# Kernel tuning notes

Measured on AMD Instinct MI355X. Metric: run time of the kernel, lower is better.

The kernel has to match this reference:

```python
import jax, jax.numpy as jnp
import numpy as np

N_NODES = 20000
N_EDGES = 640000
IN_FEATS = 128
H1, H2 = 64, 32


def setup_inputs() -> dict:
    key = jax.random.key(0)
    ks = jax.random.split(key, 7)
    features = jax.random.normal(ks[0], (N_NODES, IN_FEATS), dtype=jnp.float32)
    W1 = jax.random.normal(ks[1], (IN_FEATS, H1), dtype=jnp.float32) * (1.0 / np.sqrt(IN_FEATS))
    b1 = jax.random.normal(ks[2], (H1,), dtype=jnp.float32) * 0.01
    W2 = jax.random.normal(ks[3], (H1, H2), dtype=jnp.float32) * (1.0 / np.sqrt(H1))
    b2 = jax.random.normal(ks[4], (H2,), dtype=jnp.float32) * 0.01
    src = jax.random.randint(ks[5], (N_EDGES,), 0, N_NODES, dtype=jnp.int32)
    dst = jax.random.randint(ks[6], (N_EDGES,), 0, N_NODES, dtype=jnp.int32)
    return {"features": features, "W1": W1, "b1": b1, "W2": W2, "b2": b2,
            "src": src, "dst": dst}


def _gcn_aggregate(h, src, dst, n_nodes):
    # copy_u + sum: gather source-node features along edges, sum at destinations
    return jax.ops.segment_sum(h[src], dst, num_segments=n_nodes)


def reference(features, W1, b1, W2, b2, src, dst):
    n = features.shape[0]
    # layer 1: aggregate then linear, relu
    h = _gcn_aggregate(features, src, dst, n)          # [N, in_feats]
    x = jax.nn.relu(h @ W1 + b1)                       # [N, 64]
    # layer 2: aggregate then linear
    h2 = _gcn_aggregate(x, src, dst, n)                # [N, 64]
    return h2 @ W2 + b2                                # [N, 32]
```

## Files before the change

### kernel.cpp

```cpp
#include <hip/hip_runtime.h>


#define NF 128
#define H1 64
#define H2 32
#define CAP 128
#define CAPSH 7
#define NG8 8
#define FILL_BPG 80

__device__ __forceinline__ float blo(unsigned u) { return __uint_as_float(u << 16); }
__device__ __forceinline__ float bhi(unsigned u) { return __uint_as_float(u & 0xffff0000u); }
__device__ __forceinline__ unsigned short f2b(float f) {
    unsigned x = __float_as_uint(f);
    return (unsigned short)((x + 0x7fffu + ((x >> 16) & 1u)) >> 16);
}

__launch_bounds__(256)
__global__ void gemm1_kernel(const float* __restrict__ F, const float* __restrict__ W1,
                             unsigned short* __restrict__ P1b, int* __restrict__ cntz,
                             int n_zero, int n_nodes) {
    int idx = blockIdx.x * 256 + threadIdx.x;
    if (idx < n_zero) cntz[idx] = 0;
    __shared__ float w[NF][H1];
    const float4* w4 = (const float4*)W1;
    float4* ws4 = (float4*)&w[0][0];
#pragma unroll
    for (int j = 0; j < 8; ++j) ws4[threadIdx.x + 256 * j] = w4[threadIdx.x + 256 * j];
    __syncthreads();
    int wid = threadIdx.x >> 6, lane = threadIdx.x & 63;
#pragma unroll
    for (int r = 0; r < 8; ++r) {
        int row = blockIdx.x * 32 + wid * 8 + r;
        if (row >= n_nodes) break;
        const float4* f4 = (const float4*)(F + (size_t)row * NF);
        float acc = 0.f;
#pragma unroll
        for (int k4 = 0; k4 < NF / 4; ++k4) {
            float4 fv = f4[k4];
            acc += fv.x * w[k4 * 4 + 0][lane];
            acc += fv.y * w[k4 * 4 + 1][lane];
            acc += fv.z * w[k4 * 4 + 2][lane];
            acc += fv.w * w[k4 * 4 + 3][lane];
        }
        P1b[(size_t)row * H1 + lane] = f2b(acc);
    }
}

__launch_bounds__(256)
__global__ void stage_kernel(const int* __restrict__ src, const int* __restrict__ dst,
                             unsigned* __restrict__ staged, int* __restrict__ gcur,
                             int n_edges, int sz, int capg) {
    __shared__ int lcnt[NG8];
    __shared__ int lbase[NG8];
    int t = threadIdx.x;
    if (t < NG8) lcnt[t] = 0;
    __syncthreads();
    int i4 = (blockIdx.x * 256 + t) * 4;
    int dd[4], ss[4], bb[4], pp[4];
    if (i4 + 4 <= n_edges) {
        int4 d4 = *(const int4*)(dst + i4);
        int4 s4 = *(const int4*)(src + i4);
        dd[0] = d4.x; dd[1] = d4.y; dd[2] = d4.z; dd[3] = d4.w;
        ss[0] = s4.x; ss[1] = s4.y; ss[2] = s4.z; ss[3] = s4.w;
    } else {
#pragma unroll
        for (int k = 0; k < 4; ++k) {
            int e = i4 + k;
            dd[k] = (e < n_edges) ? dst[e] : -1;
            ss[k] = (e < n_edges) ? src[e] : 0;
        }
    }
#pragma unroll
    for (int k = 0; k < 4; ++k) {
        if (dd[k] >= 0) {
            bb[k] = (unsigned)dd[k] / (unsigned)sz;
            pp[k] = atomicAdd(&lcnt[bb[k]], 1);
        }
    }
    __syncthreads();
    if (t < NG8) lbase[t] = lcnt[t] ? atomicAdd(&gcur[t], lcnt[t]) : 0;
    __syncthreads();
#pragma unroll
    for (int k = 0; k < 4; ++k) {
        if (dd[k] >= 0) {
            int pos = lbase[bb[k]] + pp[k];
            if (pos < capg)
                staged[(size_t)bb[k] * capg + pos] = ((unsigned)dd[k] << 16) | (unsigned)ss[k];
        }
    }
}

__launch_bounds__(256)
__global__ void fill2_kernel(const unsigned* __restrict__ staged, const int* __restrict__ gcur,
                             int* __restrict__ cnt, unsigned short* __restrict__ slots,
                             int capg) {
    int g = blockIdx.x & (NG8 - 1), gi = blockIdx.x >> 3;
    int ecnt = min(gcur[g], capg);
    const unsigned* sg = staged + (size_t)g * capg;
    int stride = FILL_BPG * 256 * 4;
    for (int j = (gi * 256 + threadIdx.x) * 4; j < ecnt; j += stride) {
        if (j + 4 <= ecnt) {
            uint4 u = *(const uint4*)(sg + j);
            int d, p;
            d = u.x >> 16; p = atomicAdd(&cnt[d], 1); if (p < CAP) slots[(d << CAPSH) + p] = (unsigned short)(u.x & 0xffffu);
            d = u.y >> 16; p = atomicAdd(&cnt[d], 1); if (p < CAP) slots[(d << CAPSH) + p] = (unsigned short)(u.y & 0xffffu);
            d = u.z >> 16; p = atomicAdd(&cnt[d], 1); if (p < CAP) slots[(d << CAPSH) + p] = (unsigned short)(u.z & 0xffffu);
            d = u.w >> 16; p = atomicAdd(&cnt[d], 1); if (p < CAP) slots[(d << CAPSH) + p] = (unsigned short)(u.w & 0xffffu);
        } else {
            for (int k = j; k < ecnt; ++k) {
                unsigned u = sg[k];
                int d = u >> 16;
                int p = atomicAdd(&cnt[d], 1);
                if (p < CAP) slots[(d << CAPSH) + p] = (unsigned short)(u & 0xffffu);
            }
        }
    }
}

__launch_bounds__(256)
__global__ void agg1gemm2_kernel(const unsigned short* __restrict__ P1b,
                                 const int* __restrict__ cnt, const unsigned short* __restrict__ slots,
                                 const float* __restrict__ b1, const float* __restrict__ W2,
                                 unsigned short* __restrict__ P2b, int n_nodes, int sz) {
    __shared__ float w[H1][H2];
    __shared__ float arow[4][H1];
    const float4* w4 = (const float4*)W2;
    float4* ws4 = (float4*)&w[0][0];
#pragma unroll
    for (int j = 0; j < 2; ++j) ws4[threadIdx.x + 256 * j] = w4[threadIdx.x + 256 * j];
    __syncthreads();
    int wid = threadIdx.x >> 6, lane = threadIdx.x & 63;
    int g = blockIdx.x & (NG8 - 1), gi = blockIdx.x >> 3;
    int ni = gi * 4 + wid;
    if (ni >= sz) return;
    int node = g * sz + ni;
    if (node >= n_nodes) return;
    int deg = min(cnt[node], CAP);
    int base = node << CAPSH;
    int q = lane >> 4, c = lane & 15;
    const uint2* P1v = (const uint2*)P1b;
    float a0 = 0.f, a1 = 0.f, a2 = 0.f, a3 = 0.f;
    float c0 = 0.f, c1 = 0.f, c2 = 0.f, c3 = 0.f;
    int i = 0;
    for (; i + 8 <= deg; i += 8) {
        int sA = slots[base + i + q];
        int sB = slots[base + i + 4 + q];
        uint2 uA = P1v[(sA << 4) + c];
        uint2 uB = P1v[(sB << 4) + c];
        a0 += blo(uA.x); a1 += bhi(uA.x); a2 += blo(uA.y); a3 += bhi(uA.y);
        c0 += blo(uB.x); c1 += bhi(uB.x); c2 += blo(uB.y); c3 += bhi(uB.y);
    }
    for (; i + 4 <= deg; i += 4) {
        int sA = slots[base + i + q];
        uint2 uA = P1v[(sA << 4) + c];
        a0 += blo(uA.x); a1 += bhi(uA.x); a2 += blo(uA.y); a3 += bhi(uA.y);
    }
    int r = deg - i;
    if (q < r) {
        int sA = slots[base + i + q];
        uint2 uA = P1v[(sA << 4) + c];
        a0 += blo(uA.x); a1 += bhi(uA.x); a2 += blo(uA.y); a3 += bhi(uA.y);
    }
    a0 += c0; a1 += c1; a2 += c2; a3 += c3;
    a0 += __shfl_xor(a0, 16, 64); a0 += __shfl_xor(a0, 32, 64);
    a1 += __shfl_xor(a1, 16, 64); a1 += __shfl_xor(a1, 32, 64);
    a2 += __shfl_xor(a2, 16, 64); a2 += __shfl_xor(a2, 32, 64);
    a3 += __shfl_xor(a3, 16, 64); a3 += __shfl_xor(a3, 32, 64);
    if (q == 0) {
        float4 bb = *(const float4*)(b1 + 4 * c);
        float4 v;
        v.x = fmaxf(a0 + bb.x, 0.f);
        v.y = fmaxf(a1 + bb.y, 0.f);
        v.z = fmaxf(a2 + bb.z, 0.f);
        v.w = fmaxf(a3 + bb.w, 0.f);
        *(float4*)&arow[wid][4 * c] = v;
    }
    int half = lane >> 5, c32 = lane & 31;
    int kb = half * 32;
    float acc2 = 0.f;
#pragma unroll
    for (int k = 0; k < 32; ++k) acc2 += arow[wid][kb + k] * w[kb + k][c32];
    acc2 += __shfl_xor(acc2, 32, 64);
    if (lane < 32) P2b[(size_t)node * H2 + c32] = f2b(acc2);
}

__launch_bounds__(256)
__global__ void agg2_kernel(const unsigned short* __restrict__ P2b,
                            const int* __restrict__ cnt, const unsigned short* __restrict__ slots,
                            const float* __restrict__ b2, float* __restrict__ out,
                            int n_nodes, int sz) {
    int wid = threadIdx.x >> 6, lane = threadIdx.x & 63;
    int g = blockIdx.x & (NG8 - 1), gi = blockIdx.x >> 3;
    int ni = gi * 4 + wid;
    if (ni >= sz) return;
    int node = g * sz + ni;
    if (node >= n_nodes) return;
    int deg = min(cnt[node], CAP);
    int base = node << CAPSH;
    int o = lane >> 3, c = lane & 7;
    const uint2* P2v = (const uint2*)P2b;
    float a0 = 0.f, a1 = 0.f, a2 = 0.f, a3 = 0.f;
    float c0 = 0.f, c1 = 0.f, c2 = 0.f, c3 = 0.f;
    int i = 0;
    for (; i + 16 <= deg; i += 16) {
        int sA = slots[base + i + o];
        int sB = slots[base + i + 8 + o];
        uint2 uA = P2v[(sA << 3) + c];
        uint2 uB = P2v[(sB << 3) + c];
        a0 += blo(uA.x); a1 += bhi(uA.x); a2 += blo(uA.y); a3 += bhi(uA.y);
        c0 += blo(uB.x); c1 += bhi(uB.x); c2 += blo(uB.y); c3 += bhi(uB.y);
    }
    for (; i + 8 <= deg; i += 8) {
        int sA = slots[base + i + o];
        uint2 uA = P2v[(sA << 3) + c];
        a0 += blo(uA.x); a1 += bhi(uA.x); a2 += blo(uA.y); a3 += bhi(uA.y);
    }
    int r = deg - i;
    if (o < r) {
        int sA = slots[base + i + o];
        uint2 uA = P2v[(sA << 3) + c];
        a0 += blo(uA.x); a1 += bhi(uA.x); a2 += blo(uA.y); a3 += bhi(uA.y);
    }
    a0 += c0; a1 += c1; a2 += c2; a3 += c3;
    a0 += __shfl_xor(a0, 8, 64); a0 += __shfl_xor(a0, 16, 64); a0 += __shfl_xor(a0, 32, 64);
    a1 += __shfl_xor(a1, 8, 64); a1 += __shfl_xor(a1, 16, 64); a1 += __shfl_xor(a1, 32, 64);
    a2 += __shfl_xor(a2, 8, 64); a2 += __shfl_xor(a2, 16, 64); a2 += __shfl_xor(a2, 32, 64);
    a3 += __shfl_xor(a3, 8, 64); a3 += __shfl_xor(a3, 16, 64); a3 += __shfl_xor(a3, 32, 64);
    if (o == 0) {
        float4 bb = *(const float4*)(b2 + 4 * c);
        float4 v;
        v.x = a0 + bb.x; v.y = a1 + bb.y; v.z = a2 + bb.z; v.w = a3 + bb.w;
        *(float4*)(out + (size_t)node * H2 + 4 * c) = v;
    }
}

extern "C" void kernel_launch(void* const* d_in, const int* in_sizes, int n_in,
                              void* d_out, int out_size, void* d_ws, size_t ws_size,
                              hipStream_t stream) {
    const float* F  = (const float*)d_in[0];
    const float* W1 = (const float*)d_in[1];
    const float* b1 = (const float*)d_in[2];
    const float* W2 = (const float*)d_in[3];
    const float* b2 = (const float*)d_in[4];
    const int* src  = (const int*)d_in[5];
    const int* dst  = (const int*)d_in[6];
    float* out = (float*)d_out;

    int n_nodes = in_sizes[0] / NF;
    int n_edges = in_sizes[5];
    int sz = (n_nodes + NG8 - 1) / NG8;
    int capg = n_edges / NG8 + 8192;

    unsigned short* P1b = (unsigned short*)d_ws;
    unsigned short* P2b = P1b + (size_t)n_nodes * H1;
    unsigned short* slots = P2b + (size_t)n_nodes * H2;
    int* cnt = (int*)(slots + ((size_t)n_nodes << CAPSH));
    int* gcur = cnt + n_nodes;
    unsigned* staged = (unsigned*)(gcur + NG8);

    gemm1_kernel<<<(n_nodes + 31) / 32, 256, 0, stream>>>(F, W1, P1b, cnt,
                                                          n_nodes + NG8, n_nodes);
    stage_kernel<<<(n_edges + 1023) / 1024, 256, 0, stream>>>(src, dst, staged, gcur,
                                                              n_edges, sz, capg);
    fill2_kernel<<<FILL_BPG * NG8, 256, 0, stream>>>(staged, gcur, cnt, slots, capg);

    int bpg = (sz + 3) / 4;
    agg1gemm2_kernel<<<bpg * NG8, 256, 0, stream>>>(P1b, cnt, slots, b1, W2, P2b, n_nodes, sz);
    agg2_kernel<<<bpg * NG8, 256, 0, stream>>>(P2b, cnt, slots, b2, out, n_nodes, sz);
}
```

Before: 97.30 us.

## Fuse edge staging with gemm1 and replace global group atomics with per-chunk local sort

The edge-bucketing stage and the first dense GEMM now run as one launch, with blocks split by block index between the two roles. The staging role sorts each 1024-edge chunk by destination group in shared memory and records per-chunk group offsets, which removes the global cursor atomics and the capacity-padded buffers. The fill kernel then walks these per-chunk segments. Separately, both aggregation loops are unrolled to four independent gathers per iteration to expose more memory-level parallelism, the group index now uses a reciprocal multiply instead of an integer divide, and the GEMM inner loop's unroll is reduced to 8. The fill pass loses its vectorized uint4 loads and works on smaller segments, and the combined kernel mixes two very different block workloads.

```diff
diff --git a/kernel.cpp b/kernel.cpp
--- a/kernel.cpp
+++ b/kernel.cpp
@@ -7,113 +7,116 @@
 #define CAP 128
 #define CAPSH 7
 #define NG8 8
+#define SCHUNK 1024
 #define FILL_BPG 80
 
-__device__ __forceinline__ float blo(unsigned u) { return __uint_as_float(u << 16); }
-__device__ __forceinline__ float bhi(unsigned u) { return __uint_as_float(u & 0xffff0000u); }
-__device__ __forceinline__ unsigned short f2b(float f) {
+__device__ __forceinline__ float blo(unsigned u){ return __uint_as_float(u << 16); }
+__device__ __forceinline__ float bhi(unsigned u){ return __uint_as_float(u & 0xffff0000u); }
+__device__ __forceinline__ unsigned short f2b(float f){
     unsigned x = __float_as_uint(f);
     return (unsigned short)((x + 0x7fffu + ((x >> 16) & 1u)) >> 16);
 }
 
 __launch_bounds__(256)
-__global__ void gemm1_kernel(const float* __restrict__ F, const float* __restrict__ W1,
-                             unsigned short* __restrict__ P1b, int* __restrict__ cntz,
-                             int n_zero, int n_nodes) {
-    int idx = blockIdx.x * 256 + threadIdx.x;
-    if (idx < n_zero) cntz[idx] = 0;
-    __shared__ float w[NF][H1];
-    const float4* w4 = (const float4*)W1;
-    float4* ws4 = (float4*)&w[0][0];
-#pragma unroll
-    for (int j = 0; j < 8; ++j) ws4[threadIdx.x + 256 * j] = w4[threadIdx.x + 256 * j];
+__global__ void k1_kernel(const float* __restrict__ F, const float* __restrict__ W1,
+                          const int* __restrict__ src, const int* __restrict__ dst,
+                          unsigned* __restrict__ staged, int* __restrict__ bofs,
+                          unsigned short* __restrict__ P1b, int* __restrict__ cnt,
+                          unsigned inv_sz, int n_nodes, int n_edges, int nsb) {
+    __shared__ __align__(16) float w[NF * H1];
+    __shared__ int lcnt[NG8 + 1];
+    const int t = threadIdx.x;
+    const int bid = blockIdx.x;
+
+    if (bid < nsb) {
+        unsigned* sorted = (unsigned*)w;
+        int e0 = bid * SCHUNK;
+        int ce = min(n_edges - e0, SCHUNK);
+        if (t < NG8 + 1) lcnt[t] = 0;
+        __syncthreads();
+        int i4 = e0 + t * 4;
+        int dd[4], ss[4], bb[4], pp[4];
+        if (i4 + 4 <= n_edges) {
+            int4 d4 = *(const int4*)(dst + i4);
+            int4 s4 = *(const int4*)(src + i4);
+            dd[0]=d4.x; dd[1]=d4.y; dd[2]=d4.z; dd[3]=d4.w;
+            ss[0]=s4.x; ss[1]=s4.y; ss[2]=s4.z; ss[3]=s4.w;
+        } else {
+#pragma unroll
+            for (int k = 0; k < 4; ++k) {
+                int e = i4 + k;
+                dd[k] = (e < n_edges) ? dst[e] : -1;
+                ss[k] = (e < n_edges) ? src[e] : 0;
+            }
+        }
+#pragma unroll
+        for (int k = 0; k < 4; ++k) {
+            if (dd[k] >= 0) {
+                bb[k] = (int)(unsigned)(((unsigned long long)(unsigned)dd[k] * inv_sz) >> 32);
+                pp[k] = atomicAdd(&lcnt[bb[k]], 1);
+            }
+        }
+        __syncthreads();
+        if (t == 0) {
+            int run = 0;
+#pragma unroll
+            for (int i = 0; i < NG8 + 1; ++i) { int c = lcnt[i]; lcnt[i] = run; run += c; }
+        }
+        __syncthreads();
+#pragma unroll
+        for (int k = 0; k < 4; ++k)
+            if (dd[k] >= 0)
+                sorted[lcnt[bb[k]] + pp[k]] = ((unsigned)dd[k] << 16) | (unsigned)ss[k];
+        __syncthreads();
+        for (int j = t; j < ce; j += 256) staged[(size_t)bid * SCHUNK + j] = sorted[j];
+        if (t < NG8 + 1) bofs[t * nsb + bid] = lcnt[t];
+        return;
+    }
+
+    int gb = bid - nsb;
+    int zi = gb * 256 + t;
+    if (zi < n_nodes) cnt[zi] = 0;
+    {
+        const float4* w4 = (const float4*)W1;
+        float4* ws4 = (float4*)w;
+#pragma unroll
+        for (int j = 0; j < 8; ++j) ws4[t + 256 * j] = w4[t + 256 * j];
+    }
     __syncthreads();
-    int wid = threadIdx.x >> 6, lane = threadIdx.x & 63;
+    int wid = t >> 6, lane = t & 63;
+    int row0 = gb * 32 + wid * 8;
 #pragma unroll
     for (int r = 0; r < 8; ++r) {
-        int row = blockIdx.x * 32 + wid * 8 + r;
+        int row = row0 + r;
         if (row >= n_nodes) break;
         const float4* f4 = (const float4*)(F + (size_t)row * NF);
         float acc = 0.f;
-#pragma unroll
+#pragma unroll 8
         for (int k4 = 0; k4 < NF / 4; ++k4) {
             float4 fv = f4[k4];
-            acc += fv.x * w[k4 * 4 + 0][lane];
-            acc += fv.y * w[k4 * 4 + 1][lane];
-            acc += fv.z * w[k4 * 4 + 2][lane];
-            acc += fv.w * w[k4 * 4 + 3][lane];
+            acc += fv.x * w[(k4 * 4 + 0) * H1 + lane];
+            acc += fv.y * w[(k4 * 4 + 1) * H1 + lane];
+            acc += fv.z * w[(k4 * 4 + 2) * H1 + lane];
+            acc += fv.w * w[(k4 * 4 + 3) * H1 + lane];
         }
         P1b[(size_t)row * H1 + lane] = f2b(acc);
     }
 }
 
 __launch_bounds__(256)
-__global__ void stage_kernel(const int* __restrict__ src, const int* __restrict__ dst,
-                             unsigned* __restrict__ staged, int* __restrict__ gcur,
-                             int n_edges, int sz, int capg) {
-    __shared__ int lcnt[NG8];
-    __shared__ int lbase[NG8];
-    int t = threadIdx.x;
-    if (t < NG8) lcnt[t] = 0;
-    __syncthreads();
-    int i4 = (blockIdx.x * 256 + t) * 4;
-    int dd[4], ss[4], bb[4], pp[4];
-    if (i4 + 4 <= n_edges) {
-        int4 d4 = *(const int4*)(dst + i4);
-        int4 s4 = *(const int4*)(src + i4);
-        dd[0] = d4.x; dd[1] = d4.y; dd[2] = d4.z; dd[3] = d4.w;
-        ss[0] = s4.x; ss[1] = s4.y; ss[2] = s4.z; ss[3] = s4.w;
-    } else {
-#pragma unroll
-        for (int k = 0; k < 4; ++k) {
-            int e = i4 + k;
-            dd[k] = (e < n_edges) ? dst[e] : -1;
-            ss[k] = (e < n_edges) ? src[e] : 0;
-        }
-    }
-#pragma unroll
-    for (int k = 0; k < 4; ++k) {
-        if (dd[k] >= 0) {
-            bb[k] = (unsigned)dd[k] / (unsigned)sz;
-            pp[k] = atomicAdd(&lcnt[bb[k]], 1);
-        }
-    }
-    __syncthreads();
-    if (t < NG8) lbase[t] = lcnt[t] ? atomicAdd(&gcur[t], lcnt[t]) : 0;
-    __syncthreads();
-#pragma unroll
-    for (int k = 0; k < 4; ++k) {
-        if (dd[k] >= 0) {
-            int pos = lbase[bb[k]] + pp[k];
-            if (pos < capg)
-                staged[(size_t)bb[k] * capg + pos] = ((unsigned)dd[k] << 16) | (unsigned)ss[k];
-        }
-    }
-}
-
-__launch_bounds__(256)
-__global__ void fill2_kernel(const unsigned* __restrict__ staged, const int* __restrict__ gcur,
+__global__ void fill2_kernel(const unsigned* __restrict__ staged, const int* __restrict__ bofs,
                              int* __restrict__ cnt, unsigned short* __restrict__ slots,
-                             int capg) {
+                             int nsb) {
     int g = blockIdx.x & (NG8 - 1), gi = blockIdx.x >> 3;
-    int ecnt = min(gcur[g], capg);
-    const unsigned* sg = staged + (size_t)g * capg;
-    int stride = FILL_BPG * 256 * 4;
-    for (int j = (gi * 256 + threadIdx.x) * 4; j < ecnt; j += stride) {
-        if (j + 4 <= ecnt) {
-            uint4 u = *(const uint4*)(sg + j);
-            int d, p;
-            d = u.x >> 16; p = atomicAdd(&cnt[d], 1); if (p < CAP) slots[(d << CAPSH) + p] = (unsigned short)(u.x & 0xffffu);
-            d = u.y >> 16; p = atomicAdd(&cnt[d], 1); if (p < CAP) slots[(d << CAPSH) + p] = (unsigned short)(u.y & 0xffffu);
-            d = u.z >> 16; p = atomicAdd(&cnt[d], 1); if (p < CAP) slots[(d << CAPSH) + p] = (unsigned short)(u.z & 0xffffu);
-            d = u.w >> 16; p = atomicAdd(&cnt[d], 1); if (p < CAP) slots[(d << CAPSH) + p] = (unsigned short)(u.w & 0xffffu);
-        } else {
-            for (int k = j; k < ecnt; ++k) {
-                unsigned u = sg[k];
-                int d = u >> 16;
-                int p = atomicAdd(&cnt[d], 1);
-                if (p < CAP) slots[(d << CAPSH) + p] = (unsigned short)(u & 0xffffu);
-            }
+    for (int sb = gi; sb < nsb; sb += FILL_BPG) {
+        int st = bofs[g * nsb + sb];
+        int en = bofs[(g + 1) * nsb + sb];
+        const unsigned* seg = staged + (size_t)sb * SCHUNK;
+        for (int j = st + threadIdx.x; j < en; j += 256) {
+            unsigned u = seg[j];
+            int d = u >> 16;
+            int p = atomicAdd(&cnt[d], 1);
+            if (p < CAP) slots[(d << CAPSH) + p] = (unsigned short)(u & 0xffffu);
         }
     }
 }
@@ -123,12 +126,14 @@
                                  const int* __restrict__ cnt, const unsigned short* __restrict__ slots,
                                  const float* __restrict__ b1, const float* __restrict__ W2,
                                  unsigned short* __restrict__ P2b, int n_nodes, int sz) {
-    __shared__ float w[H1][H2];
+    __shared__ float w2s[H1 * H2];
     __shared__ float arow[4][H1];
-    const float4* w4 = (const float4*)W2;
-    float4* ws4 = (float4*)&w[0][0];
-#pragma unroll
-    for (int j = 0; j < 2; ++j) ws4[threadIdx.x + 256 * j] = w4[threadIdx.x + 256 * j];
+    {
+        const float4* w4 = (const float4*)W2;
+        float4* ws4 = (float4*)w2s;
+#pragma unroll
+        for (int j = 0; j < 2; ++j) ws4[threadIdx.x + 256 * j] = w4[threadIdx.x + 256 * j];
+    }
     __syncthreads();
     int wid = threadIdx.x >> 6, lane = threadIdx.x & 63;
     int g = blockIdx.x & (NG8 - 1), gi = blockIdx.x >> 3;
@@ -140,29 +145,34 @@
     int base = node << CAPSH;
     int q = lane >> 4, c = lane & 15;
     const uint2* P1v = (const uint2*)P1b;
-    float a0 = 0.f, a1 = 0.f, a2 = 0.f, a3 = 0.f;
-    float c0 = 0.f, c1 = 0.f, c2 = 0.f, c3 = 0.f;
+    float a0=0.f,a1=0.f,a2=0.f,a3=0.f, b0=0.f,b1v=0.f,b2v=0.f,b3=0.f;
+    float c0=0.f,c1=0.f,c2=0.f,c3=0.f, d0=0.f,d1=0.f,d2=0.f,d3=0.f;
     int i = 0;
-    for (; i + 8 <= deg; i += 8) {
+    for (; i + 16 <= deg; i += 16) {
         int sA = slots[base + i + q];
         int sB = slots[base + i + 4 + q];
+        int sC = slots[base + i + 8 + q];
+        int sD = slots[base + i + 12 + q];
         uint2 uA = P1v[(sA << 4) + c];
         uint2 uB = P1v[(sB << 4) + c];
-        a0 += blo(uA.x); a1 += bhi(uA.x); a2 += blo(uA.y); a3 += bhi(uA.y);
-        c0 += blo(uB.x); c1 += bhi(uB.x); c2 += blo(uB.y); c3 += bhi(uB.y);
+        uint2 uC = P1v[(sC << 4) + c];
+        uint2 uD = P1v[(sD << 4) + c];
+        a0 += blo(uA.x); a1 += bhi(uA.x); a2 += blo(uA.y); a3 += bhi(uA.y);
+        b0 += blo(uB.x); b1v += bhi(uB.x); b2v += blo(uB.y); b3 += bhi(uB.y);
+        c0 += blo(uC.x); c1 += bhi(uC.x); c2 += blo(uC.y); c3 += bhi(uC.y);
+        d0 += blo(uD.x); d1 += bhi(uD.x); d2 += blo(uD.y); d3 += bhi(uD.y);
     }
     for (; i + 4 <= deg; i += 4) {
         int sA = slots[base + i + q];
         uint2 uA = P1v[(sA << 4) + c];
         a0 += blo(uA.x); a1 += bhi(uA.x); a2 += blo(uA.y); a3 += bhi(uA.y);
     }
-    int r = deg - i;
-    if (q < r) {
+    if (q < deg - i) {
         int sA = slots[base + i + q];
         uint2 uA = P1v[(sA << 4) + c];
         a0 += blo(uA.x); a1 += bhi(uA.x); a2 += blo(uA.y); a3 += bhi(uA.y);
     }
-    a0 += c0; a1 += c1; a2 += c2; a3 += c3;
+    a0 += b0 + c0 + d0; a1 += b1v + c1 + d1; a2 += b2v + c2 + d2; a3 += b3 + c3 + d3;
     a0 += __shfl_xor(a0, 16, 64); a0 += __shfl_xor(a0, 32, 64);
     a1 += __shfl_xor(a1, 16, 64); a1 += __shfl_xor(a1, 32, 64);
     a2 += __shfl_xor(a2, 16, 64); a2 += __shfl_xor(a2, 32, 64);
@@ -176,11 +186,10 @@
         v.w = fmaxf(a3 + bb.w, 0.f);
         *(float4*)&arow[wid][4 * c] = v;
     }
-    int half = lane >> 5, c32 = lane & 31;
-    int kb = half * 32;
+    int half = lane >> 5, c32 = lane & 31, kb = half * 32;
     float acc2 = 0.f;
 #pragma unroll
-    for (int k = 0; k < 32; ++k) acc2 += arow[wid][kb + k] * w[kb + k][c32];
+    for (int k = 0; k < 32; ++k) acc2 += arow[wid][kb + k] * w2s[(kb + k) * H2 + c32];
     acc2 += __shfl_xor(acc2, 32, 64);
     if (lane < 32) P2b[(size_t)node * H2 + c32] = f2b(acc2);
 }
@@ -200,29 +209,34 @@
     int base = node << CAPSH;
     int o = lane >> 3, c = lane & 7;
     const uint2* P2v = (const uint2*)P2b;
-    float a0 = 0.f, a1 = 0.f, a2 = 0.f, a3 = 0.f;
-    float c0 = 0.f, c1 = 0.f, c2 = 0.f, c3 = 0.f;
+    float a0=0.f,a1=0.f,a2=0.f,a3=0.f, b0=0.f,b1v=0.f,b2v=0.f,b3=0.f;
+    float c0=0.f,c1=0.f,c2=0.f,c3=0.f, d0=0.f,d1=0.f,d2=0.f,d3=0.f;
     int i = 0;
-    for (; i + 16 <= deg; i += 16) {
+    for (; i + 32 <= deg; i += 32) {
         int sA = slots[base + i + o];
         int sB = slots[base + i + 8 + o];
+        int sC = slots[base + i + 16 + o];
+        int sD = slots[base + i + 24 + o];
         uint2 uA = P2v[(sA << 3) + c];
         uint2 uB = P2v[(sB << 3) + c];
-        a0 += blo(uA.x); a1 += bhi(uA.x); a2 += blo(uA.y); a3 += bhi(uA.y);
-        c0 += blo(uB.x); c1 += bhi(uB.x); c2 += blo(uB.y); c3 += bhi(uB.y);
+        uint2 uC = P2v[(sC << 3) + c];
+        uint2 uD = P2v[(sD << 3) + c];
+        a0 += blo(uA.x); a1 += bhi(uA.x); a2 += blo(uA.y); a3 += bhi(uA.y);
+        b0 += blo(uB.x); b1v += bhi(uB.x); b2v += blo(uB.y); b3 += bhi(uB.y);
+        c0 += blo(uC.x); c1 += bhi(uC.x); c2 += blo(uC.y); c3 += bhi(uC.y);
+        d0 += blo(uD.x); d1 += bhi(uD.x); d2 += blo(uD.y); d3 += bhi(uD.y);
     }
     for (; i + 8 <= deg; i += 8) {
         int sA = slots[base + i + o];
         uint2 uA = P2v[(sA << 3) + c];
         a0 += blo(uA.x); a1 += bhi(uA.x); a2 += blo(uA.y); a3 += bhi(uA.y);
     }
-    int r = deg - i;
-    if (o < r) {
+    if (o < deg - i) {
         int sA = slots[base + i + o];
         uint2 uA = P2v[(sA << 3) + c];
         a0 += blo(uA.x); a1 += bhi(uA.x); a2 += blo(uA.y); a3 += bhi(uA.y);
     }
-    a0 += c0; a1 += c1; a2 += c2; a3 += c3;
+    a0 += b0 + c0 + d0; a1 += b1v + c1 + d1; a2 += b2v + c2 + d2; a3 += b3 + c3 + d3;
     a0 += __shfl_xor(a0, 8, 64); a0 += __shfl_xor(a0, 16, 64); a0 += __shfl_xor(a0, 32, 64);
     a1 += __shfl_xor(a1, 8, 64); a1 += __shfl_xor(a1, 16, 64); a1 += __shfl_xor(a1, 32, 64);
     a2 += __shfl_xor(a2, 8, 64); a2 += __shfl_xor(a2, 16, 64); a2 += __shfl_xor(a2, 32, 64);
@@ -250,21 +264,20 @@
     int n_nodes = in_sizes[0] / NF;
     int n_edges = in_sizes[5];
     int sz = (n_nodes + NG8 - 1) / NG8;
-    int capg = n_edges / NG8 + 8192;
+    unsigned inv_sz = (unsigned)(((1ULL << 32) + sz - 1) / (unsigned)sz);
+    int nsb = (n_edges + SCHUNK - 1) / SCHUNK;
 
     unsigned short* P1b = (unsigned short*)d_ws;
     unsigned short* P2b = P1b + (size_t)n_nodes * H1;
     unsigned short* slots = P2b + (size_t)n_nodes * H2;
     int* cnt = (int*)(slots + ((size_t)n_nodes << CAPSH));
-    int* gcur = cnt + n_nodes;
-    unsigned* staged = (unsigned*)(gcur + NG8);
-
-    gemm1_kernel<<<(n_nodes + 31) / 32, 256, 0, stream>>>(F, W1, P1b, cnt,
-                                                          n_nodes + NG8, n_nodes);
-    stage_kernel<<<(n_edges + 1023) / 1024, 256, 0, stream>>>(src, dst, staged, gcur,
-                                                              n_edges, sz, capg);
-    fill2_kernel<<<FILL_BPG * NG8, 256, 0, stream>>>(staged, gcur, cnt, slots, capg);
-
+    unsigned* staged = (unsigned*)(cnt + n_nodes);
+    int* bofs = (int*)(staged + (size_t)nsb * SCHUNK);
+
+    int g1 = nsb + (n_nodes + 31) / 32;
+    k1_kernel<<<g1, 256, 0, stream>>>(F, W1, src, dst, staged, bofs, P1b, cnt,
+                                      inv_sz, n_nodes, n_edges, nsb);
+    fill2_kernel<<<FILL_BPG * NG8, 256, 0, stream>>>(staged, bofs, cnt, slots, nsb);
     int bpg = (sz + 3) / 4;
     agg1gemm2_kernel<<<bpg * NG8, 256, 0, stream>>>(P1b, cnt, slots, b1, W2, P2b, n_nodes, sz);
     agg2_kernel<<<bpg * NG8, 256, 0, stream>>>(P2b, cnt, slots, b2, out, n_nodes, sz);
```

Result: no change. 96.88 us (-0.4%).
